# Kernel tuning notes

Measured on AMD Instinct MI355X. Metric: run time of the kernel, lower is better.

The kernel has to match this reference:

```python
import jax, jax.numpy as jnp
import numpy as np

B, D0, D1, D2, P = 16, 2048, 4096, 4096, 64


def setup_inputs() -> dict:
    key = jax.random.key(0)
    ks = jax.random.split(key, 24)
    n = lambda k, s: jax.random.normal(k, s, dtype=jnp.float32)
    u = lambda k, s: jax.random.uniform(k, s, dtype=jnp.float32)
    return {
        'mu0': n(ks[0], (B, D0, P)),
        'lb1': n(ks[1], (B, D1)), 'ub1': n(ks[2], (B, D1)),
        'lb2': n(ks[3], (B, D2)), 'ub2': n(ks[4], (B, D2)),
        'ps1': n(ks[5], (B, D1)), 'ss1': n(ks[6], (B, D1)),
        'ps2': n(ks[7], (B, D2)), 'ss2': n(ks[8], (B, D2)),
        'mask1': u(ks[9], (B, D1)), 'mask2': u(ks[10], (B, D2)),
        'W1': n(ks[11], (D1, D0)) * 0.02, 'b1': n(ks[12], (D1,)),
        'W2': n(ks[13], (D2, D1)) * 0.02, 'b2': n(ks[14], (D2,)),
        'fc1_W': n(ks[15], (P, 5)) * 0.3, 'fc1_b': n(ks[16], (P,)) * 0.1,
        'fc11_W': n(ks[17], (P, P)) * 0.1, 'fc11_b': n(ks[18], (P,)) * 0.1,
        'fc2_W': n(ks[19], (P, 2 * P)) * 0.1, 'fc2_b': n(ks[20], (P,)) * 0.1,
        'fc21_W': n(ks[21], (P, P)) * 0.1, 'fc21_b': n(ks[22], (P,)) * 0.1,
    }


def compute_ratio(lower, upper):
    # lower - relu(lower) == min(lower, 0); relu(upper) == max(upper, 0)
    lower_temp = jnp.minimum(lower, 0.0)
    upper_temp = jnp.maximum(upper, 0.0)
    diff = upper_temp - lower_temp
    upper_ratio = upper_temp / (diff + 1e-8)
    lower_ratio = 1.0 - upper_ratio
    return upper_ratio, lower_ratio, diff


def _relu_block(pre_flat, lb, ub, ps, ss, mask,
                fc1_W, fc1_b, fc11_W, fc11_b, fc2_W, fc2_b, fc21_W, fc21_b):
    # pre_flat: [N, P] propagated neighbor embeddings; N = B * d_out
    ur, lr, diff = compute_ratio(lb.reshape(-1), ub.reshape(-1))
    info = jnp.stack([ur, lr, diff, ps.reshape(-1), ss.reshape(-1)], axis=-1)  # [N, 5]
    h = jax.nn.relu(info @ fc1_W.T + fc1_b) @ fc11_W.T + fc11_b               # [N, P]
    e = jnp.concatenate([pre_flat, h], axis=-1)                               # [N, 2P]
    out = jax.nn.relu(e @ fc2_W.T + fc2_b) @ fc21_W.T + fc21_b                # [N, P]
    return out * mask.reshape(-1, 1)


def reference(mu0, lb1, ub1, lb2, ub2, ps1, ss1, ps2, ss2, mask1, mask2,
              W1, b1, W2, b2, fc1_W, fc1_b, fc11_W, fc11_b,
              fc2_W, fc2_b, fc21_W, fc21_b):
    # Linear layer 1: W1 @ mu0 + bias (bias broadcast over embedding dim p)
    pre1 = jnp.einsum('oi,bip->bop', W1, mu0) + b1[None, :, None]  # [B, D1, P]
    mu1 = _relu_block(pre1.reshape(-1, P), lb1, ub1, ps1, ss1, mask1,
                      fc1_W, fc1_b, fc11_W, fc11_b, fc2_W, fc2_b, fc21_W, fc21_b)
    mu1 = mu1.reshape(B, D1, P)
    # Linear layer 2
    pre2 = jnp.einsum('oi,bip->bop', W2, mu1) + b2[None, :, None]  # [B, D2, P]
    mu2 = _relu_block(pre2.reshape(-1, P), lb2, ub2, ps2, ss2, mask2,
                      fc1_W, fc1_b, fc11_W, fc11_b, fc2_W, fc2_b, fc21_W, fc21_b)
    mu2 = mu2.reshape(B, D2, P)
    return jnp.stack([mu1, mu2])  # [2, B, D, P] updated embeddings
```

## Files before the change

kernel.cpp:

```cpp
#include <hip/hip_runtime.h>
#include <hip/hip_bf16.h>


#define DOUT 4096
typedef __bf16 bf16x8 __attribute__((ext_vector_type(8)));
typedef float  f32x4  __attribute__((ext_vector_type(4)));

__device__ __forceinline__ __bf16 bfc(float x) { return (__bf16)x; }

__device__ __forceinline__ bf16x8 cvt8(const float4 a, const float4 b) {
    bf16x8 r;
    r[0]=bfc(a.x); r[1]=bfc(a.y); r[2]=bfc(a.z); r[3]=bfc(a.w);
    r[4]=bfc(b.x); r[5]=bfc(b.y); r[6]=bfc(b.z); r[7]=bfc(b.w);
    return r;
}

__device__ __forceinline__ int aoff(int r, int c16) {
    return (r << 7) + ((c16 << 4) ^ ((r & 7) << 4));
}

#define WS_MU0 0
#define WS_MU1 (4u << 20)
#define WS_SM  (12u << 20)

#define BAR() asm volatile("s_barrier" ::: "memory")

__global__ __launch_bounds__(256)
void prepass_kernel(const float* __restrict__ mu0, const float* __restrict__ fc11W,
                    const float* __restrict__ fc2W, const float* __restrict__ fc21W,
                    char* __restrict__ ws)
{
    const int blk = blockIdx.x, t = threadIdx.x;
    if (blk < 512) {
        const int b = blk >> 5, kt = blk & 31;
        const int p = t & 63, kc = t >> 6;
        const float* src = mu0 + ((size_t)b * 2048 + kt * 64 + kc * 16) * 64 + p;
        char* tile = ws + WS_MU0 + ((size_t)b * 32 + kt) * 8192;
        float v[16];
        #pragma unroll
        for (int i = 0; i < 16; ++i) v[i] = src[(size_t)i * 64];
        bf16x8 o0, o1;
        #pragma unroll
        for (int i = 0; i < 8; ++i) { o0[i] = bfc(v[i]); o1[i] = bfc(v[8 + i]); }
        const int n = p >> 4, ks = kc >> 1;
        const int l0 = (((kc & 1) * 2) << 4) | (p & 15);
        const int l1 = (((kc & 1) * 2 + 1) << 4) | (p & 15);
        *(bf16x8*)(tile + ks * 4096 + n * 1024 + l0 * 16) = o0;
        *(bf16x8*)(tile + ks * 4096 + n * 1024 + l1 * 16) = o1;
    } else {
        const int idx = (blk - 512) * 256 + t;
        __bf16* dst = (__bf16*)(ws + WS_SM);
        if (idx < 4096)        dst[idx] = bfc(fc11W[idx]);
        else if (idx < 12288)  dst[idx] = bfc(fc2W[idx - 4096]);
        else                   dst[idx] = bfc(fc21W[idx - 12288]);
    }
}

#define LOADA(dst, t_) { const float* s_ = aSrc + (size_t)(t_) * 64;            \
    dst[0] = *(const float4*)s_;       dst[1] = *(const float4*)(s_ + 4);       \
    dst[2] = *(const float4*)(s_ + 8); dst[3] = *(const float4*)(s_ + 12); }

#define LOADB(dst, t_) { const char* bp_ = bW + (size_t)(t_) * 8192 + lane * 16; \
    _Pragma("unroll")                                                            \
    for (int n_ = 0; n_ < 4; ++n_) dst[n_] = *(const bf16x8*)(bp_ + n_ * 1024); }

#define MFMAS(Abuf, bset) {                                                      \
    bf16x8 af_[4];                                                               \
    _Pragma("unroll")                                                            \
    for (int m_ = 0; m_ < 4; ++m_)                                               \
        af_[m_] = *(const bf16x8*)((Abuf) + aoff(m_ * 16 + lr, khc + lg));       \
    __builtin_amdgcn_s_setprio(1);                                               \
    _Pragma("unroll")                                                            \
    for (int m_ = 0; m_ < 4; ++m_)                                               \
        _Pragma("unroll")                                                        \
        for (int n_ = 0; n_ < 4; ++n_)                                           \
            acc[m_][n_] = __builtin_amdgcn_mfma_f32_16x16x32_bf16(               \
                af_[m_], bset[n_], acc[m_][n_], 0, 0, 0);                        \
    __builtin_amdgcn_s_setprio(0); }

template <int K, bool WRITE_T>
__global__ __launch_bounds__(256, 2)
void layer_kernel(const float* __restrict__ W, const float* __restrict__ bias,
                  const char* __restrict__ wsB,
                  const float* __restrict__ lb, const float* __restrict__ ub,
                  const float* __restrict__ ps, const float* __restrict__ ss,
                  const float* __restrict__ mask,
                  const float* __restrict__ fc1W, const float* __restrict__ fc1b,
                  const __bf16* __restrict__ fc11bf, const float* __restrict__ fc11b,
                  const __bf16* __restrict__ fc2bf, const float* __restrict__ fc2b,
                  const __bf16* __restrict__ fc21bf, const float* __restrict__ fc21b,
                  float* __restrict__ out, char* __restrict__ wsT)
{
    constexpr int NT = K / 64;
    __shared__ __align__(16) char lds[49152];
    char* const pre   = lds + 32768;
    char* const T_lds = lds;
    char* const H_lds = lds + 16384;

    const int tid = threadIdx.x;
    const int lane = tid & 63, wv = tid >> 6;
    const int kh = wv >> 1, bn = wv & 1;
    const int khc = kh * 4;
    const int lr = lane & 15, lg = lane >> 4;

    const int id = blockIdx.x;
    const int vid = (id & 7) * 64 + (id >> 3);
    const int panel = vid >> 3;
    const int bgroup = vid & 7;
    const int orow0 = panel * 64;
    const int batch0 = bgroup * 2;

    const char* bW = wsB + ((size_t)(batch0 + bn) * NT) * 8192 + khc * 1024;

    const int arow = tid >> 2, aslot = tid & 3;
    const float* aSrc = W + (size_t)(orow0 + arow) * K + aslot * 16;
    const int aw0 = aoff(arow, aslot * 2);
    const int aw1 = aoff(arow, aslot * 2 + 1);
    char* const ab0 = lds;
    char* const ab1 = lds + 8192;

    const f32x4 z = {0.f, 0.f, 0.f, 0.f};
    f32x4 acc[4][4];
    #pragma unroll
    for (int m = 0; m < 4; ++m)
        #pragma unroll
        for (int n = 0; n < 4; ++n) acc[m][n] = z;

    float4 aR0[4], aR1[4];
    bf16x8 bR0[4], bR1[4];

    LOADA(aR0, 0); LOADB(bR0, 0);
    LOADA(aR1, 1); LOADB(bR1, 1);
    asm volatile("s_waitcnt vmcnt(8)" ::: "memory");
    *(bf16x8*)(ab0 + aw0) = cvt8(aR0[0], aR0[1]);
    *(bf16x8*)(ab0 + aw1) = cvt8(aR0[2], aR0[3]);
    asm volatile("s_waitcnt lgkmcnt(0)" ::: "memory");
    BAR();

    for (int t = 0; t < NT; t += 2) {
        if (t + 2 < NT) LOADA(aR0, t + 2);
        MFMAS(ab0, bR0);
        if (t + 2 < NT) LOADB(bR0, t + 2);
        if (t + 2 < NT) asm volatile("s_waitcnt vmcnt(8)" ::: "memory");
        else            asm volatile("s_waitcnt vmcnt(0)" ::: "memory");
        *(bf16x8*)(ab1 + aw0) = cvt8(aR1[0], aR1[1]);
        *(bf16x8*)(ab1 + aw1) = cvt8(aR1[2], aR1[3]);
        asm volatile("s_waitcnt lgkmcnt(0)" ::: "memory");
        BAR();
        if (t + 3 < NT) LOADA(aR1, t + 3);
        MFMAS(ab1, bR1);
        if (t + 3 < NT) LOADB(bR1, t + 3);
        if (t + 3 < NT) asm volatile("s_waitcnt vmcnt(8)" ::: "memory");
        else            asm volatile("s_waitcnt vmcnt(0)" ::: "memory");
        if (t + 2 < NT) {
            *(bf16x8*)(ab0 + aw0) = cvt8(aR0[0], aR0[1]);
            *(bf16x8*)(ab0 + aw1) = cvt8(aR0[2], aR0[3]);
        }
        asm volatile("s_waitcnt lgkmcnt(0)" ::: "memory");
        BAR();
    }
    __syncthreads();

    if (kh == 0) {
        #pragma unroll
        for (int m = 0; m < 4; ++m)
            #pragma unroll
            for (int n = 0; n < 4; ++n)
                *(f32x4*)(lds + bn * 16384 + ((m * 4 + n) * 64 + lane) * 16) = acc[m][n];
    }
    __syncthreads();
    if (kh == 1) {
        #pragma unroll
        for (int m = 0; m < 4; ++m)
            #pragma unroll
            for (int n = 0; n < 4; ++n)
                acc[m][n] += *(const f32x4*)(lds + bn * 16384 + ((m * 4 + n) * 64 + lane) * 16);
        char* const dst = pre + bn * 8192;
        #pragma unroll
        for (int m = 0; m < 4; ++m)
            #pragma unroll
            for (int n = 0; n < 4; ++n) {
                const int col = n * 16 + lr;
                #pragma unroll
                for (int r = 0; r < 4; ++r) {
                    const int row = m * 16 + lg * 4 + r;
                    const float bs = bias[orow0 + row];
                    *(__bf16*)(dst + row * 128 + ((2 * col) ^ ((row & 7) << 4))) =
                        bfc(acc[m][n][r] + bs);
                }
            }
    }
    __syncthreads();

    const int wm = wv >> 1, wn = wv & 1;

    {
        const int row = tid >> 1;
        const int j0 = (tid & 1) * 32;
        const int bb = batch0 + (row >> 6);
        const int g = bb * DOUT + orow0 + (row & 63);
        const float lv = lb[g], uv = ub[g];
        const float lt = fminf(lv, 0.f), ut = fmaxf(uv, 0.f);
        const float diff = ut - lt;
        const float urr = ut / (diff + 1e-8f);
        const float lrr = 1.f - urr, i3 = ps[g], i4 = ss[g];
        #pragma unroll
        for (int c = 0; c < 4; ++c) {
            bf16x8 v;
            #pragma unroll
            for (int jj = 0; jj < 8; ++jj) {
                const int j = j0 + c * 8 + jj;
                const float* w = fc1W + j * 5;
                const float tv = fc1b[j] + urr * w[0] + lrr * w[1] + diff * w[2]
                               + i3 * w[3] + i4 * w[4];
                v[jj] = bfc(fmaxf(tv, 0.f));
            }
            *(bf16x8*)(T_lds + aoff(row, (j0 >> 3) + c)) = v;
        }
    }
    __syncthreads();

    {
        f32x4 hacc[4][2];
        #pragma unroll
        for (int m = 0; m < 4; ++m) { hacc[m][0] = z; hacc[m][1] = z; }
        #pragma unroll
        for (int ks = 0; ks < 2; ++ks) {
            bf16x8 a[4];
            #pragma unroll
            for (int m = 0; m < 4; ++m)
                a[m] = *(const bf16x8*)(T_lds + aoff(wm * 64 + m * 16 + lr, ks * 4 + lg));
            #pragma unroll
            for (int n = 0; n < 2; ++n) {
                const int j = wn * 32 + n * 16 + lr;
                const bf16x8 bw = *(const bf16x8*)(fc11bf + (size_t)j * 64 + ks * 32 + lg * 8);
                #pragma unroll
                for (int m = 0; m < 4; ++m)
                    hacc[m][n] = __builtin_amdgcn_mfma_f32_16x16x32_bf16(a[m], bw, hacc[m][n], 0, 0, 0);
            }
        }
        char* const Hq = H_lds + wm * 8192;
        #pragma unroll
        for (int n = 0; n < 2; ++n) {
            const int j = wn * 32 + n * 16 + lr;
            const float bj = fc11b[j];
            #pragma unroll
            for (int m = 0; m < 4; ++m)
                #pragma unroll
                for (int r = 0; r < 4; ++r) {
                    const int row = m * 16 + lg * 4 + r;
                    *(__bf16*)(Hq + row * 128 + ((2 * j) ^ ((row & 7) << 4))) =
                        bfc(hacc[m][n][r] + bj);
                }
        }
    }
    __syncthreads();

    {
        f32x4 uacc[4][2];
        #pragma unroll
        for (int m = 0; m < 4; ++m) { uacc[m][0] = z; uacc[m][1] = z; }
        #pragma unroll
        for (int ks = 0; ks < 4; ++ks) {
            const char* base = ((ks < 2) ? pre : H_lds) + wm * 8192;
            const int kb = ((ks & 1) * 64 + lg * 16);
            bf16x8 a[4];
            #pragma unroll
            for (int m = 0; m < 4; ++m) {
                const int row = m * 16 + lr;
                a[m] = *(const bf16x8*)(base + row * 128 + (kb ^ ((row & 7) << 4)));
            }
            #pragma unroll
            for (int n = 0; n < 2; ++n) {
                const int j = wn * 32 + n * 16 + lr;
                const bf16x8 bw = *(const bf16x8*)(fc2bf + (size_t)j * 128 + ks * 32 + lg * 8);
                #pragma unroll
                for (int m = 0; m < 4; ++m)
                    uacc[m][n] = __builtin_amdgcn_mfma_f32_16x16x32_bf16(a[m], bw, uacc[m][n], 0, 0, 0);
            }
        }
        __syncthreads();
        #pragma unroll
        for (int n = 0; n < 2; ++n) {
            const int j = wn * 32 + n * 16 + lr;
            const float bj = fc2b[j];
            #pragma unroll
            for (int m = 0; m < 4; ++m)
                #pragma unroll
                for (int r = 0; r < 4; ++r) {
                    const int row = wm * 64 + m * 16 + lg * 4 + r;
                    *(__bf16*)(T_lds + row * 128 + ((2 * j) ^ ((row & 7) << 4))) =
                        bfc(fmaxf(uacc[m][n][r] + bj, 0.f));
                }
        }
    }
    __syncthreads();

    {
        f32x4 oacc[4][2];
        #pragma unroll
        for (int m = 0; m < 4; ++m) { oacc[m][0] = z; oacc[m][1] = z; }
        #pragma unroll
        for (int ks = 0; ks < 2; ++ks) {
            bf16x8 a[4];
            #pragma unroll
            for (int m = 0; m < 4; ++m)
                a[m] = *(const bf16x8*)(T_lds + aoff(wm * 64 + m * 16 + lr, ks * 4 + lg));
            #pragma unroll
            for (int n = 0; n < 2; ++n) {
                const int j = wn * 32 + n * 16 + lr;
                const bf16x8 bw = *(const bf16x8*)(fc21bf + (size_t)j * 64 + ks * 32 + lg * 8);
                #pragma unroll
                for (int m = 0; m < 4; ++m)
                    oacc[m][n] = __builtin_amdgcn_mfma_f32_16x16x32_bf16(a[m], bw, oacc[m][n], 0, 0, 0);
            }
        }
        const int bb = batch0 + wm;
        #pragma unroll
        for (int n = 0; n < 2; ++n) {
            const int j = wn * 32 + n * 16 + lr;
            const float bj = fc21b[j];
            #pragma unroll
            for (int m = 0; m < 4; ++m)
                #pragma unroll
                for (int r = 0; r < 4; ++r) {
                    const int row = m * 16 + lg * 4 + r;
                    const int g = bb * DOUT + orow0 + row;
                    const float o = (oacc[m][n][r] + bj) * mask[g];
                    out[(size_t)g * 64 + j] = o;
                    if (WRITE_T)
                        *(__bf16*)(H_lds + wm * 8192 + j * 128 +
                                   ((2 * row) ^ ((j & 7) << 4))) = bfc(o);
                }
        }
    }
    if (WRITE_T) {
        __syncthreads();
        #pragma unroll
        for (int i = 0; i < 4; ++i) {
            const int idx = i * 256 + tid;
            const int qq = idx >> 9, rr = idx & 511;
            const int ks = rr >> 8, n = (rr >> 6) & 3, ln = rr & 63;
            const int j = n * 16 + (ln & 15);
            const int k = ks * 32 + (ln >> 4) * 8;
            const bf16x8 v = *(const bf16x8*)(H_lds + qq * 8192 + j * 128 +
                                              ((2 * k) ^ ((j & 7) << 4)));
            const int bb = batch0 + qq;
            *(bf16x8*)(wsT + ((size_t)bb * 64 + panel) * 8192 +
                       ks * 4096 + n * 1024 + ln * 16) = v;
        }
    }
}

extern "C" void kernel_launch(void* const* d_in, const int* in_sizes, int n_in,
                              void* d_out, int out_size, void* d_ws, size_t ws_size,
                              hipStream_t stream) {
    const float* mu0   = (const float*)d_in[0];
    const float* lb1   = (const float*)d_in[1];
    const float* ub1   = (const float*)d_in[2];
    const float* lb2   = (const float*)d_in[3];
    const float* ub2   = (const float*)d_in[4];
    const float* ps1   = (const float*)d_in[5];
    const float* ss1   = (const float*)d_in[6];
    const float* ps2   = (const float*)d_in[7];
    const float* ss2   = (const float*)d_in[8];
    const float* mask1 = (const float*)d_in[9];
    const float* mask2 = (const float*)d_in[10];
    const float* W1    = (const float*)d_in[11];
    const float* b1    = (const float*)d_in[12];
    const float* W2    = (const float*)d_in[13];
    const float* b2    = (const float*)d_in[14];
    const float* fc1W  = (const float*)d_in[15];
    const float* fc1b  = (const float*)d_in[16];
    const float* fc11W = (const float*)d_in[17];
    const float* fc11b = (const float*)d_in[18];
    const float* fc2W  = (const float*)d_in[19];
    const float* fc2b  = (const float*)d_in[20];
    const float* fc21W = (const float*)d_in[21];
    const float* fc21b = (const float*)d_in[22];

    char* ws = (char*)d_ws;
    float* mu1 = (float*)d_out;
    float* mu2 = (float*)d_out + (size_t)16 * 4096 * 64;
    const __bf16* fc11bf = (const __bf16*)(ws + WS_SM);
    const __bf16* fc2bf  = (const __bf16*)(ws + WS_SM) + 4096;
    const __bf16* fc21bf = (const __bf16*)(ws + WS_SM) + 12288;

    prepass_kernel<<<576, 256, 0, stream>>>(mu0, fc11W, fc2W, fc21W, ws);

    layer_kernel<2048, true><<<512, 256, 0, stream>>>(
        W1, b1, ws + WS_MU0, lb1, ub1, ps1, ss1, mask1,
        fc1W, fc1b, fc11bf, fc11b, fc2bf, fc2b, fc21bf, fc21b,
        mu1, ws + WS_MU1);

    layer_kernel<4096, false><<<512, 256, 0, stream>>>(
        W2, b2, ws + WS_MU1, lb2, ub2, ps2, ss2, mask2,
        fc1W, fc1b, fc11bf, fc11b, fc2bf, fc2b, fc21bf, fc21b,
        mu2, nullptr);
}
```

Measured before the change: 118.1 us.

## Stagger K-tile start per block, coalesce W loads, raise occupancy to three blocks

Each block now begins its K loop at a block-dependent offset and wraps around, so concurrent blocks read different parts of W and the shared B tiles at once. The W load mapping changes from 16 consecutive floats per thread to 4-float chunks across 16 threads per row, with four row strides, giving more coalesced loads and 8-byte swizzled LDS writes. The launch bound rises to 3 blocks per CU. The loop no longer has tail guards and always prefetches wrapped tiles, which adds redundant loads at the end and may cause register spills under the tighter budget.

```diff
diff --git a/kernel.cpp b/kernel.cpp
--- a/kernel.cpp
+++ b/kernel.cpp
@@ -4,6 +4,7 @@
 
 #define DOUT 4096
 typedef __bf16 bf16x8 __attribute__((ext_vector_type(8)));
+typedef __bf16 bf16x4 __attribute__((ext_vector_type(4)));
 typedef float  f32x4  __attribute__((ext_vector_type(4)));
 
 __device__ __forceinline__ __bf16 bfc(float x) { return (__bf16)x; }
@@ -14,6 +15,11 @@
     r[4]=bfc(b.x); r[5]=bfc(b.y); r[6]=bfc(b.z); r[7]=bfc(b.w);
     return r;
 }
+__device__ __forceinline__ bf16x4 cvt4(const float4 a) {
+    bf16x4 r;
+    r[0]=bfc(a.x); r[1]=bfc(a.y); r[2]=bfc(a.z); r[3]=bfc(a.w);
+    return r;
+}
 
 __device__ __forceinline__ int aoff(int r, int c16) {
     return (r << 7) + ((c16 << 4) ^ ((r & 7) << 4));
@@ -22,8 +28,6 @@
 #define WS_MU0 0
 #define WS_MU1 (4u << 20)
 #define WS_SM  (12u << 20)
-
-#define BAR() asm volatile("s_barrier" ::: "memory")
 
 __global__ __launch_bounds__(256)
 void prepass_kernel(const float* __restrict__ mu0, const float* __restrict__ fc11W,
@@ -56,11 +60,19 @@
     }
 }
 
-#define LOADA(dst, t_) { const float* s_ = aSrc + (size_t)(t_) * 64;            \
-    dst[0] = *(const float4*)s_;       dst[1] = *(const float4*)(s_ + 4);       \
-    dst[2] = *(const float4*)(s_ + 8); dst[3] = *(const float4*)(s_ + 12); }
-
-#define LOADB(dst, t_) { const char* bp_ = bW + (size_t)(t_) * 8192 + lane * 16; \
+#define LOADA(dst, kt_) { const float* s_ = aSrc + (size_t)(kt_) * 64;          \
+    dst[0] = *(const float4*)s_;                                                \
+    dst[1] = *(const float4*)(s_ + 16 * K);                                     \
+    dst[2] = *(const float4*)(s_ + 32 * K);                                     \
+    dst[3] = *(const float4*)(s_ + 48 * K); }
+
+#define WRITEA(buf, set) {                                                      \
+    *(bf16x4*)((buf) + awb)        = cvt4(set[0]);                              \
+    *(bf16x4*)((buf) + awb + 2048) = cvt4(set[1]);                              \
+    *(bf16x4*)((buf) + awb + 4096) = cvt4(set[2]);                              \
+    *(bf16x4*)((buf) + awb + 6144) = cvt4(set[3]); }
+
+#define LOADB(dst, kt_) { const char* bp_ = bW + (size_t)(kt_) * 8192 + lane * 16; \
     _Pragma("unroll")                                                            \
     for (int n_ = 0; n_ < 4; ++n_) dst[n_] = *(const bf16x8*)(bp_ + n_ * 1024); }
 
@@ -79,7 +91,7 @@
     __builtin_amdgcn_s_setprio(0); }
 
 template <int K, bool WRITE_T>
-__global__ __launch_bounds__(256, 2)
+__global__ __launch_bounds__(256, 3)
 void layer_kernel(const float* __restrict__ W, const float* __restrict__ bias,
                   const char* __restrict__ wsB,
                   const float* __restrict__ lb, const float* __restrict__ ub,
@@ -112,12 +124,12 @@
 
     const char* bW = wsB + ((size_t)(batch0 + bn) * NT) * 8192 + khc * 1024;
 
-    const int arow = tid >> 2, aslot = tid & 3;
-    const float* aSrc = W + (size_t)(orow0 + arow) * K + aslot * 16;
-    const int aw0 = aoff(arow, aslot * 2);
-    const int aw1 = aoff(arow, aslot * 2 + 1);
-    char* const ab0 = lds;
-    char* const ab1 = lds + 8192;
+    const int arow = tid >> 4, acol = tid & 15;
+    const float* aSrc = W + (size_t)(orow0 + arow) * K + acol * 4;
+    const int awb = arow * 128 + ((acol * 8) ^ ((arow & 7) << 4));
+
+    const int t0 = vid & (NT - 1);
+#define KT(i_) ((t0 + (i_)) & (NT - 1))
 
     const f32x4 z = {0.f, 0.f, 0.f, 0.f};
     f32x4 acc[4][4];
@@ -129,35 +141,28 @@
     float4 aR0[4], aR1[4];
     bf16x8 bR0[4], bR1[4];
 
-    LOADA(aR0, 0); LOADB(bR0, 0);
-    LOADA(aR1, 1); LOADB(bR1, 1);
+    LOADA(aR0, KT(0)); LOADB(bR0, KT(0));
+    LOADA(aR1, KT(1)); LOADB(bR1, KT(1));
     asm volatile("s_waitcnt vmcnt(8)" ::: "memory");
-    *(bf16x8*)(ab0 + aw0) = cvt8(aR0[0], aR0[1]);
-    *(bf16x8*)(ab0 + aw1) = cvt8(aR0[2], aR0[3]);
+    WRITEA(lds, aR0);
     asm volatile("s_waitcnt lgkmcnt(0)" ::: "memory");
-    BAR();
+    asm volatile("s_barrier" ::: "memory");
 
     for (int t = 0; t < NT; t += 2) {
-        if (t + 2 < NT) LOADA(aR0, t + 2);
-        MFMAS(ab0, bR0);
-        if (t + 2 < NT) LOADB(bR0, t + 2);
-        if (t + 2 < NT) asm volatile("s_waitcnt vmcnt(8)" ::: "memory");
-        else            asm volatile("s_waitcnt vmcnt(0)" ::: "memory");
-        *(bf16x8*)(ab1 + aw0) = cvt8(aR1[0], aR1[1]);
-        *(bf16x8*)(ab1 + aw1) = cvt8(aR1[2], aR1[3]);
+        LOADA(aR0, KT(t + 2));
+        MFMAS(lds, bR0);
+        LOADB(bR0, KT(t + 2));
+        asm volatile("s_waitcnt vmcnt(8)" ::: "memory");
+        WRITEA(lds + 8192, aR1);
         asm volatile("s_waitcnt lgkmcnt(0)" ::: "memory");
-        BAR();
-        if (t + 3 < NT) LOADA(aR1, t + 3);
-        MFMAS(ab1, bR1);
-        if (t + 3 < NT) LOADB(bR1, t + 3);
-        if (t + 3 < NT) asm volatile("s_waitcnt vmcnt(8)" ::: "memory");
-        else            asm volatile("s_waitcnt vmcnt(0)" ::: "memory");
-        if (t + 2 < NT) {
-            *(bf16x8*)(ab0 + aw0) = cvt8(aR0[0], aR0[1]);
-            *(bf16x8*)(ab0 + aw1) = cvt8(aR0[2], aR0[3]);
-        }
+        asm volatile("s_barrier" ::: "memory");
+        LOADA(aR1, KT(t + 3));
+        MFMAS(lds + 8192, bR1);
+        LOADB(bR1, KT(t + 3));
+        asm volatile("s_waitcnt vmcnt(8)" ::: "memory");
+        WRITEA(lds, aR0);
         asm volatile("s_waitcnt lgkmcnt(0)" ::: "memory");
-        BAR();
+        asm volatile("s_barrier" ::: "memory");
     }
     __syncthreads();
 
@@ -350,6 +355,7 @@
                        ks * 4096 + n * 1024 + ln * 16) = v;
         }
     }
+#undef KT
 }
 
 extern "C" void kernel_launch(void* const* d_in, const int* in_sizes, int n_in,
```

Result: slower. 173.9 us (+47.3%).
